# Performance work log

Hardware: AMD Instinct MI355X
Metric: run time of the kernel (lower is better)

Reference implementation:

```python
import jax, jax.numpy as jnp
import numpy as np
import math

STEP_SIZE = 1.0


def setup_inputs() -> dict:
    key = jax.random.key(0)
    ks = jax.random.split(key, 6)
    B, L, C, H, O = 4096, 256, 8, 128, 1
    n_int = L - 1
    coeffs = jax.random.normal(ks[0], (B, n_int, 4 * C), dtype=jnp.float32) * 0.1

    def lin(k, i, o):
        kw, kb = jax.random.split(k)
        s = 1.0 / math.sqrt(i)
        W = jax.random.uniform(kw, (i, o), minval=-s, maxval=s, dtype=jnp.float32)
        b = jax.random.uniform(kb, (o,), minval=-s, maxval=s, dtype=jnp.float32)
        return W, b

    W_init, b_init = lin(ks[1], C, H)
    W1, b1 = lin(ks[2], H, H)
    W2, b2 = lin(ks[3], H, H)
    W3, b3 = lin(ks[4], H, H * C)
    W_out, b_out = lin(ks[5], H, O)
    return dict(coeffs=coeffs, W_init=W_init, b_init=b_init, W1=W1, b1=b1,
                W2=W2, b2=b2, W3=W3, b3=b3, W_out=W_out, b_out=b_out)


def reference(coeffs, W_init, b_init, W1, b1, W2, b2, W3, b3, W_out, b_out):
    B, n_int, four_c = coeffs.shape
    C = four_c // 4
    H = W1.shape[0]
    # torchcde CubicSpline coefficient layout: a, b, two_c, three_d
    a, bcoef, two_c, three_d = jnp.split(coeffs, 4, axis=-1)  # each (B, n_int, C)
    knots = jnp.arange(n_int + 1, dtype=coeffs.dtype)  # t = linspace(0, n_int, n_int+1)
    T = float(n_int)

    def X_deriv(t):
        # torchcde _interpret_t: bucketize(t, knots)-1 clamped; here knots uniform
        idx = jnp.clip(jnp.searchsorted(knots, t, side='left') - 1, 0, n_int - 1)
        frac = t - knots[idx]
        return bcoef[:, idx] + (two_c[:, idx] + three_d[:, idx] * frac) * frac  # (B, C)

    def ode_f(t, z):
        # CDEFunc: Linear->Softplus x2, Linear->Tanh, reshape to (B, H, C)
        h = jax.nn.softplus(z @ W1 + b1)
        h = jax.nn.softplus(h @ W2 + b2)
        f = jnp.tanh(h @ W3 + b3).reshape(B, H, C)
        return jnp.einsum('bhc,bc->bh', f, X_deriv(t))  # f(z) @ dX/dt

    # torchdiffeq fixed-grid rk4 with step_size (3/8 rule: rk4_alt_step_func)
    n_steps = int(math.ceil(T / STEP_SIZE))
    ts = jnp.minimum(jnp.arange(n_steps + 1, dtype=coeffs.dtype) * STEP_SIZE, T)
    t0s, dts = ts[:-1], ts[1:] - ts[:-1]

    z0 = a[:, 0] @ W_init + b_init  # X.evaluate(interval[0]) == a at first knot

    def step(z, td):
        t0, dt = td
        k1 = ode_f(t0, z)
        k2 = ode_f(t0 + dt / 3, z + dt * k1 / 3)
        k3 = ode_f(t0 + dt * 2 / 3, z + dt * (k2 - k1 / 3))
        k4 = ode_f(t0 + dt, z + dt * (k1 - k2 + k3))
        return z + dt * (k1 + 3.0 * (k2 + k3) + k4) / 8.0, None

    zT, _ = jax.lax.scan(step, z0, (t0s, dts))
    return zT @ W_out + b_out
```

## Files before the change

### kernel.cpp

```cpp
#include <hip/hip_runtime.h>

#define NINT  255
#define BM    16
#define PITCH 136

typedef __bf16 bf16x8 __attribute__((ext_vector_type(8)));
typedef float  f32x4  __attribute__((ext_vector_type(4)));

#define MFMA(a, b, c) __builtin_amdgcn_mfma_f32_16x16x32_bf16((a), (b), (c), 0, 0, 0)

__device__ __forceinline__ unsigned short f2b(float f) {
    __bf16 b = (__bf16)f;
    return __builtin_bit_cast(unsigned short, b);
}

__device__ __forceinline__ float sp_f(float x) {
    float e = __builtin_amdgcn_exp2f(x * 1.4426950408889634f);
    float y = __builtin_amdgcn_logf(1.0f + e) * 0.6931471805599453f;
    return (x > 80.0f) ? x : y;
}

__device__ __forceinline__ float tanh_f(float x) {
    float e = __builtin_amdgcn_exp2f(x * 2.8853900817779268f);
    float r = __builtin_amdgcn_rcpf(e + 1.0f);
    return fmaf(-2.0f, r, 1.0f);
}

__global__ void prep_frags(const float* __restrict__ W1, const float* __restrict__ W2,
                           const float* __restrict__ W3,
                           unsigned short* __restrict__ W1f, unsigned short* __restrict__ W2f,
                           unsigned short* __restrict__ W3f) {
    const int e = blockIdx.x * 256 + threadIdx.x;
    const int i = e & 7;
    const int l = (e >> 3) & 63;
    const int t = (e >> 9) & 3;
    const int n = e >> 11;
    const int k = 32 * t + ((l >> 4) & 3) * 8 + i;
    const int c = l & 15;
    if (e < 16384) {
        W1f[e] = f2b(W1[k * 128 + 16 * n + c]);
        W2f[e] = f2b(W2[k * 128 + 16 * n + c]);
    }
    W3f[e] = f2b(W3[k * 1024 + 16 * n + c]);
}

#define STAGE_BODY(ST, XD)                                                       \
{                                                                                \
    bf16x8 a0[4];                                                                \
    _Pragma("unroll")                                                            \
    for (int t = 0; t < 4; ++t)                                                  \
        a0[t] = *(const bf16x8*)(Zs + batch * PITCH + t * 32 + koff);            \
    f32x4 h1 = {b1r, b1r, b1r, b1r};                                             \
    _Pragma("unroll")                                                            \
    for (int t = 0; t < 4; ++t) h1 = MFMA(a0[t], w1r[t], h1);                    \
    _Pragma("unroll")                                                            \
    for (int i = 0; i < 4; ++i)                                                  \
        H1s[(g * 4 + i) * PITCH + 16 * w + batch] = f2b(sp_f(h1[i]));            \
    __syncthreads();                                                             \
    bf16x8 a1[4];                                                                \
    _Pragma("unroll")                                                            \
    for (int t = 0; t < 4; ++t)                                                  \
        a1[t] = *(const bf16x8*)(H1s + batch * PITCH + t * 32 + koff);           \
    f32x4 h2 = {b2r, b2r, b2r, b2r};                                             \
    _Pragma("unroll")                                                            \
    for (int t = 0; t < 4; ++t) h2 = MFMA(a1[t], w2r[t], h2);                    \
    _Pragma("unroll")                                                            \
    for (int i = 0; i < 4; ++i)                                                  \
        H2s[(g * 4 + i) * PITCH + 16 * w + batch] = f2b(sp_f(h2[i]));            \
    __syncthreads();                                                             \
    bf16x8 bfr[4];                                                               \
    _Pragma("unroll")                                                            \
    for (int t = 0; t < 4; ++t)                                                  \
        bfr[t] = *(const bf16x8*)(H2s + batch * PITCH + t * 32 + koff);          \
    f32x4 acc[8];                                                                \
    _Pragma("unroll")                                                            \
    for (int jl = 0; jl < 4; ++jl) {                                             \
        acc[jl] = MFMA(w3g[jl][0], bfr[0], b3r8[jl]);                            \
        _Pragma("unroll")                                                        \
        for (int t = 1; t < 4; ++t) acc[jl] = MFMA(w3g[jl][t], bfr[t], acc[jl]); \
    }                                                                            \
    _Pragma("unroll")                                                            \
    for (int jl = 4; jl < 8; ++jl) {                                             \
        acc[jl] = MFMA(w3rv[(((jl - 4) * 8 + w) * 4 + 0) * 64 + l], bfr[0], b3r8[jl]); \
        _Pragma("unroll")                                                        \
        for (int t = 1; t < 4; ++t)                                              \
            acc[jl] = MFMA(w3rv[(((jl - 4) * 8 + w) * 4 + t) * 64 + l], bfr[t], acc[jl]); \
    }                                                                            \
    _Pragma("unroll")                                                            \
    for (int jl = 0; jl < 8; ++jl) {                                             \
        float p = 0.0f;                                                          \
        _Pragma("unroll")                                                        \
        for (int i = 0; i < 4; ++i) p = fmaf(tanh_f(acc[jl][i]), (XD)[i], p);    \
        p += __shfl_xor(p, 16, 64);                                              \
        float znew;                                                              \
        if (ST == 0)      { k1r[jl] = p; znew = zb[jl] + p * (1.0f/3.0f); }      \
        else if (ST == 1) { k2r[jl] = p; znew = zb[jl] + p - k1r[jl] * (1.0f/3.0f); } \
        else if (ST == 2) { k3r[jl] = p; znew = zb[jl] + k1r[jl] - k2r[jl] + p; } \
        else { zb[jl] = fmaf(k1r[jl] + 3.0f*(k2r[jl] + k3r[jl]) + p, 0.125f, zb[jl]); znew = zb[jl]; } \
        if ((g & 1) == 0)                                                        \
            Zs[batch * PITCH + 16 * jl + 2 * w + hb] = f2b(znew);                \
    }                                                                            \
    __syncthreads();                                                             \
}

__global__ __launch_bounds__(512, 2)
void cde_mfma(const float* __restrict__ coeffs,
              const float* __restrict__ W_init, const float* __restrict__ b_init,
              const float* __restrict__ b1, const float* __restrict__ b2,
              const float* __restrict__ b3,
              const float* __restrict__ W_out, const float* __restrict__ b_out,
              const unsigned short* __restrict__ w1f, const unsigned short* __restrict__ w2f,
              const unsigned short* __restrict__ w3f,
              float* __restrict__ out)
{
    __shared__ __align__(16) unsigned short W3r_lds[65536];
    __shared__ __align__(16) unsigned short Zs [BM * PITCH];
    __shared__ __align__(16) unsigned short H1s[BM * PITCH];
    __shared__ __align__(16) unsigned short H2s[BM * PITCH];
    __shared__ __align__(16) float Outp[16][16];

    const int tid     = threadIdx.x;
    const int rowbase = blockIdx.x * BM;
    const int l       = tid & 63;
    const int w       = tid >> 6;
    const int batch   = l & 15;
    const int g       = (l >> 4) & 3;
    const int hb      = g >> 1;
    const int chB     = 4 * (g & 1);
    const int koff    = g * 8;

    for (int k4 = tid; k4 < 8192; k4 += 512)
        ((uint4*)W3r_lds)[k4] = ((const uint4*)(w3f + 32 * 2048))[k4];

    const bf16x8* w1v = (const bf16x8*)w1f;
    const bf16x8* w2v = (const bf16x8*)w2f;
    const bf16x8* w3v = (const bf16x8*)w3f;
    bf16x8 w1r[4], w2r[4], w3g[4][4];
    #pragma unroll
    for (int t = 0; t < 4; ++t) {
        w1r[t] = w1v[(w * 4 + t) * 64 + l];
        w2r[t] = w2v[(w * 4 + t) * 64 + l];
    }
    #pragma unroll
    for (int jl = 0; jl < 4; ++jl)
        #pragma unroll
        for (int t = 0; t < 4; ++t)
            w3g[jl][t] = w3v[((8 * jl + w) * 4 + t) * 64 + l];

    const float b1r = b1[16 * w + batch];
    const float b2r = b2[16 * w + batch];
    f32x4 b3r8[8];
    #pragma unroll
    for (int jl = 0; jl < 8; ++jl)
        b3r8[jl] = *(const f32x4*)&b3[16 * (8 * jl + w) + 4 * g];

    float zb[8], k1r[8], k2r[8], k3r[8];
    {
        const float* ap = coeffs + (size_t)(rowbase + batch) * (NINT * 32);
        float av[8];
        #pragma unroll
        for (int c = 0; c < 8; ++c) av[c] = ap[c];
        #pragma unroll
        for (int jl = 0; jl < 8; ++jl) {
            const int h = 16 * jl + 2 * w + hb;
            float z = b_init[h];
            #pragma unroll
            for (int c = 0; c < 8; ++c) z = fmaf(av[c], W_init[c * 128 + h], z);
            zb[jl] = z;
            if ((g & 1) == 0) Zs[batch * PITCH + h] = f2b(z);
        }
    }

    const float* cpx = coeffs + (size_t)(rowbase + batch) * (NINT * 32) + chB;
    f32x4 bB  = *(const f32x4*)(cpx + 8);
    f32x4 tcv = *(const f32x4*)(cpx + 16);
    f32x4 tdv = *(const f32x4*)(cpx + 24);
    f32x4 xd0 = bB;

    const bf16x8* w3rv = (const bf16x8*)W3r_lds;
    __syncthreads();

    #pragma unroll 1
    for (int step = 0; step < NINT; ++step) {
        const int nxt = (step + 1 < NINT) ? step + 1 : NINT - 1;
        const float* cn = cpx + nxt * 32;
        const f32x4 nbB = *(const f32x4*)(cn + 8);
        const f32x4 ntc = *(const f32x4*)(cn + 16);
        const f32x4 ntd = *(const f32x4*)(cn + 24);

        STAGE_BODY(0, xd0)

        f32x4 xd1, xd2, xd3;
        #pragma unroll
        for (int i = 0; i < 4; ++i) {
            xd1[i] = bB[i] + (tcv[i] + tdv[i] * (1.0f/3.0f)) * (1.0f/3.0f);
            xd2[i] = bB[i] + (tcv[i] + tdv[i] * (2.0f/3.0f)) * (2.0f/3.0f);
            xd3[i] = bB[i] + tcv[i] + tdv[i];
        }

        STAGE_BODY(1, xd1)
        STAGE_BODY(2, xd2)
        STAGE_BODY(3, xd3)

        xd0 = xd3;
        bB = nbB; tcv = ntc; tdv = ntd;
    }

    if ((g & 1) == 0) {
        float prt = 0.0f;
        #pragma unroll
        for (int jl = 0; jl < 8; ++jl)
            prt = fmaf(zb[jl], W_out[16 * jl + 2 * w + hb], prt);
        Outp[2 * w + hb][batch] = prt;
    }
    __syncthreads();
    if (tid < 16) {
        float s = b_out[0];
        #pragma unroll
        for (int p = 0; p < 16; ++p) s += Outp[p][tid];
        out[rowbase + tid] = s;
    }
}

extern "C" void kernel_launch(void* const* d_in, const int* in_sizes, int n_in,
                              void* d_out, int out_size, void* d_ws, size_t ws_size,
                              hipStream_t stream) {
    const float* coeffs = (const float*)d_in[0];
    const float* W_init = (const float*)d_in[1];
    const float* b_init = (const float*)d_in[2];
    const float* W1     = (const float*)d_in[3];
    const float* b1     = (const float*)d_in[4];
    const float* W2     = (const float*)d_in[5];
    const float* b2     = (const float*)d_in[6];
    const float* W3     = (const float*)d_in[7];
    const float* b3     = (const float*)d_in[8];
    const float* W_out  = (const float*)d_in[9];
    const float* b_out  = (const float*)d_in[10];
    float* outp = (float*)d_out;

    unsigned short* w1f = (unsigned short*)d_ws;
    unsigned short* w2f = w1f + 16384;
    unsigned short* w3f = w2f + 16384;

    hipLaunchKernelGGL(prep_frags, dim3(512), dim3(256), 0, stream, W1, W2, W3, w1f, w2f, w3f);
    hipLaunchKernelGGL(cde_mfma, dim3(4096 / BM), dim3(512), 0, stream,
                       coeffs, W_init, b_init, b1, b2, b3, W_out, b_out,
                       w1f, w2f, w3f, outp);
}
```

Before: 2.550 ms.

## Double workgroup to 16 waves, split W3 columns and stage W1/W2 in LDS

Launches 1024-thread blocks so the W3 GEMM and tanh/contraction epilogue are spread over 16 waves with 4 column groups each, instead of 8 waves with 8. W1/W2 fragments and b3 move into LDS to free registers, and only the last quarter of W3 stays in LDS. Waves 8-15 sit idle during the two small hidden layers. Next-interval coefficient loads are no longer issued ahead of the four stages. The aim is more latency hiding and less per-thread register pressure in a serial, latency-bound RK4 loop, at the cost of partly idle waves and extra LDS reads for weights.

```diff
diff --git a/kernel.cpp b/kernel.cpp
--- a/kernel.cpp
+++ b/kernel.cpp
@@ -44,66 +44,69 @@
     W3f[e] = f2b(W3[k * 1024 + 16 * n + c]);
 }
 
-#define STAGE_BODY(ST, XD)                                                       \
+#define STAGE_BODY(ST)                                                           \
 {                                                                                \
-    bf16x8 a0[4];                                                                \
-    _Pragma("unroll")                                                            \
-    for (int t = 0; t < 4; ++t)                                                  \
-        a0[t] = *(const bf16x8*)(Zs + batch * PITCH + t * 32 + koff);            \
-    f32x4 h1 = {b1r, b1r, b1r, b1r};                                             \
-    _Pragma("unroll")                                                            \
-    for (int t = 0; t < 4; ++t) h1 = MFMA(a0[t], w1r[t], h1);                    \
-    _Pragma("unroll")                                                            \
-    for (int i = 0; i < 4; ++i)                                                  \
-        H1s[(g * 4 + i) * PITCH + 16 * w + batch] = f2b(sp_f(h1[i]));            \
-    __syncthreads();                                                             \
-    bf16x8 a1[4];                                                                \
-    _Pragma("unroll")                                                            \
-    for (int t = 0; t < 4; ++t)                                                  \
-        a1[t] = *(const bf16x8*)(H1s + batch * PITCH + t * 32 + koff);           \
-    f32x4 h2 = {b2r, b2r, b2r, b2r};                                             \
-    _Pragma("unroll")                                                            \
-    for (int t = 0; t < 4; ++t) h2 = MFMA(a1[t], w2r[t], h2);                    \
-    _Pragma("unroll")                                                            \
-    for (int i = 0; i < 4; ++i)                                                  \
-        H2s[(g * 4 + i) * PITCH + 16 * w + batch] = f2b(sp_f(h2[i]));            \
-    __syncthreads();                                                             \
-    bf16x8 bfr[4];                                                               \
-    _Pragma("unroll")                                                            \
-    for (int t = 0; t < 4; ++t)                                                  \
-        bfr[t] = *(const bf16x8*)(H2s + batch * PITCH + t * 32 + koff);          \
-    f32x4 acc[8];                                                                \
-    _Pragma("unroll")                                                            \
-    for (int jl = 0; jl < 4; ++jl) {                                             \
-        acc[jl] = MFMA(w3g[jl][0], bfr[0], b3r8[jl]);                            \
-        _Pragma("unroll")                                                        \
-        for (int t = 1; t < 4; ++t) acc[jl] = MFMA(w3g[jl][t], bfr[t], acc[jl]); \
-    }                                                                            \
-    _Pragma("unroll")                                                            \
-    for (int jl = 4; jl < 8; ++jl) {                                             \
-        acc[jl] = MFMA(w3rv[(((jl - 4) * 8 + w) * 4 + 0) * 64 + l], bfr[0], b3r8[jl]); \
-        _Pragma("unroll")                                                        \
-        for (int t = 1; t < 4; ++t)                                              \
-            acc[jl] = MFMA(w3rv[(((jl - 4) * 8 + w) * 4 + t) * 64 + l], bfr[t], acc[jl]); \
-    }                                                                            \
-    _Pragma("unroll")                                                            \
-    for (int jl = 0; jl < 8; ++jl) {                                             \
-        float p = 0.0f;                                                          \
-        _Pragma("unroll")                                                        \
-        for (int i = 0; i < 4; ++i) p = fmaf(tanh_f(acc[jl][i]), (XD)[i], p);    \
-        p += __shfl_xor(p, 16, 64);                                              \
-        float znew;                                                              \
-        if (ST == 0)      { k1r[jl] = p; znew = zb[jl] + p * (1.0f/3.0f); }      \
-        else if (ST == 1) { k2r[jl] = p; znew = zb[jl] + p - k1r[jl] * (1.0f/3.0f); } \
-        else if (ST == 2) { k3r[jl] = p; znew = zb[jl] + k1r[jl] - k2r[jl] + p; } \
-        else { zb[jl] = fmaf(k1r[jl] + 3.0f*(k2r[jl] + k3r[jl]) + p, 0.125f, zb[jl]); znew = zb[jl]; } \
-        if ((g & 1) == 0)                                                        \
-            Zs[batch * PITCH + 16 * jl + 2 * w + hb] = f2b(znew);                \
+    if (w < 8) {                                                                 \
+        bf16x8 a0[4];                                                            \
+        _Pragma("unroll") for (int t = 0; t < 4; ++t)                            \
+            a0[t] = *(const bf16x8*)(Zs + l15 * PITCH + t * 32 + koff);          \
+        f32x4 h1 = {b1r, b1r, b1r, b1r};                                         \
+        _Pragma("unroll") for (int t = 0; t < 4; ++t)                            \
+            h1 = MFMA(a0[t], wf1[(w * 4 + t) * 64 + l], h1);                     \
+        _Pragma("unroll") for (int i = 0; i < 4; ++i)                            \
+            H1s[(g * 4 + i) * PITCH + 16 * w + l15] = f2b(sp_f(h1[i]));          \
     }                                                                            \
     __syncthreads();                                                             \
-}
-
-__global__ __launch_bounds__(512, 2)
+    if (w < 8) {                                                                 \
+        bf16x8 a1[4];                                                            \
+        _Pragma("unroll") for (int t = 0; t < 4; ++t)                            \
+            a1[t] = *(const bf16x8*)(H1s + l15 * PITCH + t * 32 + koff);         \
+        f32x4 h2 = {b2r, b2r, b2r, b2r};                                         \
+        _Pragma("unroll") for (int t = 0; t < 4; ++t)                            \
+            h2 = MFMA(a1[t], wf2[(w * 4 + t) * 64 + l], h2);                     \
+        _Pragma("unroll") for (int i = 0; i < 4; ++i)                            \
+            H2s[(g * 4 + i) * PITCH + 16 * w + l15] = f2b(sp_f(h2[i]));          \
+    }                                                                            \
+    __syncthreads();                                                             \
+    {                                                                            \
+        bf16x8 bfr[4];                                                           \
+        _Pragma("unroll") for (int t = 0; t < 4; ++t)                            \
+            bfr[t] = *(const bf16x8*)(H2s + l15 * PITCH + t * 32 + koff);        \
+        f32x4 acc[4];                                                            \
+        _Pragma("unroll") for (int jl = 0; jl < 3; ++jl) {                       \
+            acc[jl] = *(const f32x4*)&b3s[16 * (16 * jl + w) + 4 * g];           \
+            _Pragma("unroll") for (int t = 0; t < 4; ++t)                        \
+                acc[jl] = MFMA(w3g[jl][t], bfr[t], acc[jl]);                     \
+        }                                                                        \
+        acc[3] = *(const f32x4*)&b3s[16 * (48 + w) + 4 * g];                     \
+        _Pragma("unroll") for (int t = 0; t < 4; ++t)                            \
+            acc[3] = MFMA(w3lv[(w * 4 + t) * 64 + l], bfr[t], acc[3]);           \
+        f32x4 xdv;                                                               \
+        if (ST == 0) xdv = xd0;                                                  \
+        else if (ST == 1) { _Pragma("unroll") for (int i = 0; i < 4; ++i)        \
+            xdv[i] = bB[i] + (tcv[i] + tdv[i] * (1.0f/3.0f)) * (1.0f/3.0f); }    \
+        else if (ST == 2) { _Pragma("unroll") for (int i = 0; i < 4; ++i)        \
+            xdv[i] = bB[i] + (tcv[i] + tdv[i] * (2.0f/3.0f)) * (2.0f/3.0f); }    \
+        else { _Pragma("unroll") for (int i = 0; i < 4; ++i)                     \
+            xdv[i] = bB[i] + tcv[i] + tdv[i];  xd0 = xdv; }                      \
+        _Pragma("unroll") for (int jl = 0; jl < 4; ++jl) {                       \
+            float p = 0.0f;                                                      \
+            _Pragma("unroll") for (int i = 0; i < 4; ++i)                        \
+                p = fmaf(tanh_f(acc[jl][i]), xdv[i], p);                         \
+            p += __shfl_xor(p, 16, 64);                                          \
+            float znew;                                                          \
+            if (ST == 0)      { k1r[jl] = p; znew = zb[jl] + p * (1.0f/3.0f); }  \
+            else if (ST == 1) { k2r[jl] = p; znew = zb[jl] + p - k1r[jl] * (1.0f/3.0f); } \
+            else if (ST == 2) { k3r[jl] = p; znew = zb[jl] + k1r[jl] - k2r[jl] + p; } \
+            else { zb[jl] = fmaf(k1r[jl] + 3.0f*(k2r[jl] + k3r[jl]) + p, 0.125f, zb[jl]); znew = zb[jl]; } \
+            if ((g & 1) == 0)                                                    \
+                Zs[l15 * PITCH + ((jl < 3) ? 32 * jl : 96) + h2wb] = f2b(znew);  \
+        }                                                                        \
+    }                                                                            \
+    __syncthreads();                                                             \
+}
+
+__global__ __launch_bounds__(1024, 4)
 void cde_mfma(const float* __restrict__ coeffs,
               const float* __restrict__ W_init, const float* __restrict__ b_init,
               const float* __restrict__ b1, const float* __restrict__ b2,
@@ -113,111 +116,98 @@
               const unsigned short* __restrict__ w3f,
               float* __restrict__ out)
 {
-    __shared__ __align__(16) unsigned short W3r_lds[65536];
+    __shared__ __align__(16) unsigned short W1f_lds[16384];
+    __shared__ __align__(16) unsigned short W2f_lds[16384];
+    __shared__ __align__(16) unsigned short W3l_lds[32768];
     __shared__ __align__(16) unsigned short Zs [BM * PITCH];
     __shared__ __align__(16) unsigned short H1s[BM * PITCH];
     __shared__ __align__(16) unsigned short H2s[BM * PITCH];
-    __shared__ __align__(16) float Outp[16][16];
+    __shared__ __align__(16) float b3s[1024];
+    __shared__ __align__(16) float Outp[32][16];
 
     const int tid     = threadIdx.x;
     const int rowbase = blockIdx.x * BM;
     const int l       = tid & 63;
     const int w       = tid >> 6;
-    const int batch   = l & 15;
+    const int l15     = l & 15;
     const int g       = (l >> 4) & 3;
     const int hb      = g >> 1;
     const int chB     = 4 * (g & 1);
     const int koff    = g * 8;
-
-    for (int k4 = tid; k4 < 8192; k4 += 512)
-        ((uint4*)W3r_lds)[k4] = ((const uint4*)(w3f + 32 * 2048))[k4];
-
-    const bf16x8* w1v = (const bf16x8*)w1f;
-    const bf16x8* w2v = (const bf16x8*)w2f;
+    const int h2wb    = 2 * w + hb;
+
+    for (int k4 = tid; k4 < 2048; k4 += 1024) {
+        ((uint4*)W1f_lds)[k4] = ((const uint4*)w1f)[k4];
+        ((uint4*)W2f_lds)[k4] = ((const uint4*)w2f)[k4];
+    }
+    for (int k4 = tid; k4 < 4096; k4 += 1024)
+        ((uint4*)W3l_lds)[k4] = ((const uint4*)(w3f + 48 * 2048))[k4];
+    if (tid < 1024) b3s[tid] = b3[tid];
+
     const bf16x8* w3v = (const bf16x8*)w3f;
-    bf16x8 w1r[4], w2r[4], w3g[4][4];
+    bf16x8 w3g[3][4];
     #pragma unroll
-    for (int t = 0; t < 4; ++t) {
-        w1r[t] = w1v[(w * 4 + t) * 64 + l];
-        w2r[t] = w2v[(w * 4 + t) * 64 + l];
-    }
-    #pragma unroll
-    for (int jl = 0; jl < 4; ++jl)
+    for (int jl = 0; jl < 3; ++jl)
         #pragma unroll
         for (int t = 0; t < 4; ++t)
-            w3g[jl][t] = w3v[((8 * jl + w) * 4 + t) * 64 + l];
-
-    const float b1r = b1[16 * w + batch];
-    const float b2r = b2[16 * w + batch];
-    f32x4 b3r8[8];
-    #pragma unroll
-    for (int jl = 0; jl < 8; ++jl)
-        b3r8[jl] = *(const f32x4*)&b3[16 * (8 * jl + w) + 4 * g];
-
-    float zb[8], k1r[8], k2r[8], k3r[8];
+            w3g[jl][t] = w3v[((16 * jl + w) * 4 + t) * 64 + l];
+
+    const float b1r = b1[16 * (w & 7) + l15];
+    const float b2r = b2[16 * (w & 7) + l15];
+
+    float zb[4], k1r[4], k2r[4], k3r[4];
     {
-        const float* ap = coeffs + (size_t)(rowbase + batch) * (NINT * 32);
+        const float* ap = coeffs + (size_t)(rowbase + l15) * (NINT * 32);
         float av[8];
         #pragma unroll
         for (int c = 0; c < 8; ++c) av[c] = ap[c];
         #pragma unroll
-        for (int jl = 0; jl < 8; ++jl) {
-            const int h = 16 * jl + 2 * w + hb;
+        for (int jl = 0; jl < 4; ++jl) {
+            const int h = ((jl < 3) ? 32 * jl : 96) + h2wb;
             float z = b_init[h];
             #pragma unroll
             for (int c = 0; c < 8; ++c) z = fmaf(av[c], W_init[c * 128 + h], z);
             zb[jl] = z;
-            if ((g & 1) == 0) Zs[batch * PITCH + h] = f2b(z);
+            if ((g & 1) == 0) Zs[l15 * PITCH + h] = f2b(z);
         }
     }
 
-    const float* cpx = coeffs + (size_t)(rowbase + batch) * (NINT * 32) + chB;
+    const float* cpx = coeffs + (size_t)(rowbase + l15) * (NINT * 32) + chB;
     f32x4 bB  = *(const f32x4*)(cpx + 8);
     f32x4 tcv = *(const f32x4*)(cpx + 16);
     f32x4 tdv = *(const f32x4*)(cpx + 24);
     f32x4 xd0 = bB;
 
-    const bf16x8* w3rv = (const bf16x8*)W3r_lds;
+    const bf16x8* wf1  = (const bf16x8*)W1f_lds;
+    const bf16x8* wf2  = (const bf16x8*)W2f_lds;
+    const bf16x8* w3lv = (const bf16x8*)W3l_lds;
     __syncthreads();
 
     #pragma unroll 1
     for (int step = 0; step < NINT; ++step) {
+        STAGE_BODY(0)
+        STAGE_BODY(1)
+        STAGE_BODY(2)
+        STAGE_BODY(3)
         const int nxt = (step + 1 < NINT) ? step + 1 : NINT - 1;
         const float* cn = cpx + nxt * 32;
-        const f32x4 nbB = *(const f32x4*)(cn + 8);
-        const f32x4 ntc = *(const f32x4*)(cn + 16);
-        const f32x4 ntd = *(const f32x4*)(cn + 24);
-
-        STAGE_BODY(0, xd0)
-
-        f32x4 xd1, xd2, xd3;
-        #pragma unroll
-        for (int i = 0; i < 4; ++i) {
-            xd1[i] = bB[i] + (tcv[i] + tdv[i] * (1.0f/3.0f)) * (1.0f/3.0f);
-            xd2[i] = bB[i] + (tcv[i] + tdv[i] * (2.0f/3.0f)) * (2.0f/3.0f);
-            xd3[i] = bB[i] + tcv[i] + tdv[i];
-        }
-
-        STAGE_BODY(1, xd1)
-        STAGE_BODY(2, xd2)
-        STAGE_BODY(3, xd3)
-
-        xd0 = xd3;
-        bB = nbB; tcv = ntc; tdv = ntd;
+        bB  = *(const f32x4*)(cn + 8);
+        tcv = *(const f32x4*)(cn + 16);
+        tdv = *(const f32x4*)(cn + 24);
     }
 
     if ((g & 1) == 0) {
         float prt = 0.0f;
         #pragma unroll
-        for (int jl = 0; jl < 8; ++jl)
-            prt = fmaf(zb[jl], W_out[16 * jl + 2 * w + hb], prt);
-        Outp[2 * w + hb][batch] = prt;
+        for (int jl = 0; jl < 4; ++jl)
+            prt = fmaf(zb[jl], W_out[((jl < 3) ? 32 * jl : 96) + h2wb], prt);
+        Outp[h2wb][l15] = prt;
     }
     __syncthreads();
     if (tid < 16) {
         float s = b_out[0];
         #pragma unroll
-        for (int p = 0; p < 16; ++p) s += Outp[p][tid];
+        for (int p = 0; p < 32; ++p) s += Outp[p][tid];
         out[rowbase + tid] = s;
     }
 }
@@ -243,7 +233,7 @@
     unsigned short* w3f = w2f + 16384;
 
     hipLaunchKernelGGL(prep_frags, dim3(512), dim3(256), 0, stream, W1, W2, W3, w1f, w2f, w3f);
-    hipLaunchKernelGGL(cde_mfma, dim3(4096 / BM), dim3(512), 0, stream,
+    hipLaunchKernelGGL(cde_mfma, dim3(4096 / BM), dim3(1024), 0, stream,
                        coeffs, W_init, b_init, b1, b2, b3, W_out, b_out,
                        w1f, w2f, w3f, outp);
 }
```

Result: slower. 3.111 ms (+22.0%).
